# Kernel tuning notes

Measured on AMD Instinct MI355X. Metric: run time of the kernel, lower is better.

The kernel has to match this reference:

```python
import jax, jax.numpy as jnp
import numpy as np
from jax import lax

NUM_HEADS = 8
NUM_SELECTS = 10
CLIP = 10.0  # tanh logit clipping in pointer-style SingleHeadAttention
NEG = -1e9   # finite -inf substitute (safe under autodiff)


def setup_inputs() -> dict:
    key = jax.random.key(0)
    ks = jax.random.split(key, 8)
    B, N, D = 64, 2048, 256
    s = 1.0 / np.sqrt(D)
    return {
        "encoder_output": jax.random.normal(ks[0], (B, N, D), jnp.float32),
        "in_proj_w": jax.random.uniform(ks[1], (3 * D, D), jnp.float32, -s, s),
        "in_proj_b": jnp.zeros((3 * D,), jnp.float32),
        "out_w": jax.random.uniform(ks[2], (D, D), jnp.float32, -s, s),
        "out_b": jnp.zeros((D,), jnp.float32),
        "sha_wq": jax.random.uniform(ks[3], (D, D), jnp.float32, -s, s),
        "sha_wk": jax.random.uniform(ks[4], (D, D), jnp.float32, -s, s),
        "is_training": False,
    }


def reference(encoder_output, in_proj_w, in_proj_b, out_w, out_b, sha_wq, sha_wk, is_training):
    B, N, D = encoder_output.shape
    H, dh, S = NUM_HEADS, D // NUM_HEADS, NUM_SELECTS
    Wq, Wk, Wv = in_proj_w[:D], in_proj_w[D:2 * D], in_proj_w[2 * D:]
    bq, bk, bv = in_proj_b[:D], in_proj_b[D:2 * D], in_proj_b[2 * D:]

    h_mean = jnp.mean(encoder_output, axis=1)                         # [B,D]
    # MHA query is constant across steps; K/V projections of the encoder too.
    q = (h_mean @ Wq.T + bq).reshape(B, H, dh)                        # [B,H,dh]
    k = (encoder_output @ Wk.T + bk).reshape(B, N, H, dh)             # [B,N,H,dh]
    v = (encoder_output @ Wv.T + bv).reshape(B, N, H, dh)             # [B,N,H,dh]
    ksingle = encoder_output @ sha_wk.T                               # [B,N,D]
    scale = 1.0 / np.sqrt(dh)
    scale2 = 1.0 / np.sqrt(D)
    bidx = jnp.arange(B)

    def step(mask, _):
        # multi-head cross attention, key_padding_mask = mask
        s_mha = jnp.einsum('bhd,bnhd->bhn', q, k) * scale             # [B,H,N]
        s_mha = jnp.where(mask[:, None, :], NEG, s_mha)
        a = jax.nn.softmax(s_mha, axis=-1)
        ctx = jnp.einsum('bhn,bnhd->bhd', a, v).reshape(B, D)
        attn_out = ctx @ out_w.T + out_b                              # [B,D]
        # single-head pointer attention with tanh clipping
        qs = attn_out @ sha_wq.T                                      # [B,D]
        u = CLIP * jnp.tanh(jnp.einsum('bd,bnd->bn', qs, ksingle) * scale2)
        u = jnp.where(mask, NEG, u)                                   # [B,N]
        logp = jax.nn.log_softmax(u, axis=-1)
        p = jnp.exp(logp)
        ent = -jnp.sum(jnp.where(p > 0, p * logp, 0.0), axis=-1)
        # is_training=False path: greedy argmax (deterministic reference)
        idx = jnp.argmax(p, axis=-1)                                  # [B]
        pi_s = p[bidx, idx]
        new_mask = mask.at[bidx, idx].set(True)
        return new_mask, (idx, pi_s, ent)

    mask0 = jnp.zeros((B, N), dtype=bool)
    _, (idxs, pis, ents) = lax.scan(step, mask0, None, length=S)
    selected_clients = idxs.T.astype(jnp.int64 if jax.config.jax_enable_x64 else jnp.int32)  # [B,S]
    pi = pis.T                                                        # [B,S]
    entropy = jnp.sum(ents, axis=0)                                   # [B]
    return selected_clients, pi, entropy
```

## Files before the change

kernel.cpp:

```cpp
#include <hip/hip_runtime.h>
#include <hip/hip_bf16.h>
#include <math.h>

namespace {
constexpr int Bc = 64, Nc = 2048, Dc = 256, Hc = 8, DHc = 32, Sc = 10;
constexpr float kNeg = -1000000000.0f;
constexpr float kClip = 10.0f;
constexpr float kScale = 0.17677669529663687f;
constexpr float kScale2 = 0.0625f;
}

__global__ __launch_bounds__(256) void k_hmean_part(const float* __restrict__ enc,
                                                    float* __restrict__ hpart) {
  int b = blockIdx.x >> 5, c = blockIdx.x & 31, d = threadIdx.x;
  const float* p = enc + ((size_t)b * Nc + c * 64) * Dc + d;
  float s = 0.f;
  #pragma unroll 8
  for (int n = 0; n < 64; ++n) s += p[(size_t)n * Dc];
  hpart[(size_t)blockIdx.x * Dc + d] = s;
}

__global__ __launch_bounds__(256) void k_qgc(const float* __restrict__ hpart,
                                             const float* __restrict__ w_in,
                                             const float* __restrict__ b_in,
                                             float* __restrict__ g, float* __restrict__ c) {
  int b = blockIdx.x, t = threadIdx.x;
  __shared__ float hm[Dc];
  __shared__ float qsh[Dc];
  {
    float s = 0.f;
    for (int cc = 0; cc < 32; ++cc) s += hpart[(size_t)(b * 32 + cc) * Dc + t];
    hm[t] = s * (1.0f / Nc);
  }
  __syncthreads();
  {
    const float* row = w_in + (size_t)t * Dc;
    float acc = b_in[t];
    for (int d = 0; d < Dc; ++d) acc += row[d] * hm[d];
    qsh[t] = acc;
  }
  __syncthreads();
  for (int h = 0; h < Hc; ++h) {
    float acc = 0.f;
    const float* wk = w_in + (size_t)(Dc + h * DHc) * Dc + t;
    const float* qh = qsh + h * DHc;
    #pragma unroll 8
    for (int i = 0; i < DHc; ++i) acc += qh[i] * wk[(size_t)i * Dc];
    g[((size_t)b * Hc + h) * Dc + t] = acc;
  }
  if (t < Hc) {
    float acc = 0.f;
    for (int i = 0; i < DHc; ++i) acc += qsh[t * DHc + i] * b_in[Dc + t * DHc + i];
    c[b * Hc + t] = acc;
  }
}

__global__ __launch_bounds__(256) void k_A1(const float* __restrict__ swq,
                                            const float* __restrict__ ow,
                                            const float* __restrict__ ob,
                                            float* __restrict__ M1, float* __restrict__ m1b) {
  int i = blockIdx.x, e = threadIdx.x;
  __shared__ float row[Dc];
  __shared__ float red[256];
  row[e] = swq[(size_t)i * Dc + e];
  __syncthreads();
  float acc = 0.f;
  #pragma unroll 4
  for (int k = 0; k < Dc; ++k) acc += row[k] * ow[(size_t)k * Dc + e];
  M1[(size_t)i * Dc + e] = acc;
  red[e] = row[e] * ob[e];
  __syncthreads();
  for (int off = 128; off >= 1; off >>= 1) {
    if (e < off) red[e] += red[e + off];
    __syncthreads();
  }
  if (e == 0) m1b[i] = red[0];
}

__global__ __launch_bounds__(256) void k_A2(const float* __restrict__ swk,
                                            const float* __restrict__ M1,
                                            const float* __restrict__ m1b,
                                            const float* __restrict__ b_in,
                                            float* __restrict__ Aout, float* __restrict__ cvec) {
  int d = blockIdx.x, e = threadIdx.x;
  __shared__ float col[Dc];
  __shared__ float red[256];
  col[e] = swk[(size_t)e * Dc + d];
  __syncthreads();
  float acc = 0.f;
  #pragma unroll 4
  for (int k = 0; k < Dc; ++k) acc += col[k] * M1[(size_t)k * Dc + e];
  Aout[(size_t)d * Dc + e] = acc;
  red[e] = acc * b_in[2 * Dc + e] + col[e] * m1b[e];
  __syncthreads();
  for (int off = 128; off >= 1; off >>= 1) {
    if (e < off) red[e] += red[e + off];
    __syncthreads();
  }
  if (e == 0) cvec[d] = red[0];
}

__global__ __launch_bounds__(256) void k_A3(const float* __restrict__ Aout,
                                            const float* __restrict__ w_in,
                                            float* __restrict__ BT) {
  int h = blockIdx.x >> 3, et = blockIdx.x & 7, d = threadIdx.x;
  float arow[DHc];
  #pragma unroll
  for (int i = 0; i < DHc; ++i) arow[i] = Aout[(size_t)d * Dc + h * DHc + i];
  __shared__ float wv[DHc][DHc];
  for (int k = threadIdx.x; k < DHc * DHc; k += 256) {
    int i = k >> 5, j = k & 31;
    wv[i][j] = w_in[(size_t)(2 * Dc + h * DHc + i) * Dc + et * DHc + j];
  }
  __syncthreads();
  for (int j = 0; j < DHc; ++j) {
    float acc = 0.f;
    #pragma unroll
    for (int i = 0; i < DHc; ++i) acc += arow[i] * wv[i][j];
    BT[((size_t)h * Dc + et * DHc + j) * Dc + d] = acc;
  }
}

__global__ __launch_bounds__(256) void k_scores(const float* __restrict__ enc,
                                                const float* __restrict__ g,
                                                const float* __restrict__ c,
                                                float* __restrict__ s) {
  int b = blockIdx.x >> 4, nt = blockIdx.x & 15, t = threadIdx.x;
  __shared__ __align__(16) float gsm[Hc * Dc];
  __shared__ float csm[Hc];
  for (int k = t; k < Hc * Dc; k += 256) gsm[k] = g[(size_t)b * Hc * Dc + k];
  if (t < Hc) csm[t] = c[b * Hc + t];
  __syncthreads();
  int row = t >> 1, half = t & 1;
  int n = nt * 128 + row;
  const float4* rowp = reinterpret_cast<const float4*>(enc + ((size_t)b * Nc + n) * Dc);
  float acc[Hc] = {};
  #pragma unroll 8
  for (int i = 0; i < 32; ++i) {
    int d4 = i * 2 + half;
    const float4 e = rowp[d4];
    #pragma unroll
    for (int h = 0; h < Hc; ++h) {
      const float4 g4 = *reinterpret_cast<const float4*>(gsm + h * Dc + d4 * 4);
      acc[h] += e.x * g4.x + e.y * g4.y + e.z * g4.z + e.w * g4.w;
    }
  }
  #pragma unroll
  for (int h = 0; h < Hc; ++h) acc[h] += __shfl_xor(acc[h], 1);
  if (half == 0) {
    #pragma unroll
    for (int h = 0; h < Hc; ++h)
      s[((size_t)b * Hc + h) * Nc + n] = kScale * (acc[h] + csm[h]);
  }
}

__global__ __launch_bounds__(256) void k_rowmax(const float* __restrict__ s,
                                                float* __restrict__ mrow) {
  int bh = blockIdx.x, t = threadIdx.x;
  __shared__ float red[256];
  float m = -3.0e38f;
  #pragma unroll
  for (int q = 0; q < 8; ++q) m = fmaxf(m, s[(size_t)bh * Nc + q * 256 + t]);
  red[t] = m;
  __syncthreads();
  for (int off = 128; off >= 1; off >>= 1) {
    if (t < off) red[t] = fmaxf(red[t], red[t + off]);
    __syncthreads();
  }
  if (t == 0) mrow[bh] = red[0];
}

__global__ __launch_bounds__(256) void k_S0part(const float* __restrict__ enc,
                                                const float* __restrict__ s,
                                                const float* __restrict__ mrow,
                                                float* __restrict__ w,
                                                float* __restrict__ Spart) {
  int b = blockIdx.x >> 3, cid = blockIdx.x & 7, t = threadIdx.x;
  __shared__ float wsm[Hc * 256];
  #pragma unroll
  for (int h = 0; h < Hc; ++h) {
    float m = mrow[b * Hc + h];
    float e = expf(s[((size_t)b * Hc + h) * Nc + cid * 256 + t] - m);
    wsm[h * 256 + t] = e;
    w[((size_t)b * Hc + h) * Nc + cid * 256 + t] = e;
  }
  __syncthreads();
  float acc[Hc] = {};
  const float* ep = enc + ((size_t)b * Nc + cid * 256) * Dc + t;
  for (int ni = 0; ni < 256; ++ni) {
    float ev = ep[(size_t)ni * Dc];
    #pragma unroll
    for (int h = 0; h < Hc; ++h) acc[h] += wsm[h * 256 + ni] * ev;
  }
  #pragma unroll
  for (int h = 0; h < Hc; ++h)
    Spart[(((size_t)b * 8 + cid) * Hc + h) * Dc + t] = acc[h];
}

__global__ __launch_bounds__(256) void k_S0red(const float* __restrict__ Spart,
                                               const float* __restrict__ w,
                                               float* __restrict__ Sacc,
                                               float* __restrict__ W0) {
  int b = blockIdx.x >> 3, h = blockIdx.x & 7, t = threadIdx.x;
  __shared__ float red[256];
  float acc = 0.f;
  for (int cid = 0; cid < 8; ++cid)
    acc += Spart[(((size_t)b * 8 + cid) * Hc + h) * Dc + t];
  Sacc[((size_t)b * Hc + h) * Dc + t] = acc;
  float ws = 0.f;
  #pragma unroll
  for (int q = 0; q < 8; ++q) ws += w[((size_t)b * Hc + h) * Nc + q * 256 + t];
  red[t] = ws;
  __syncthreads();
  for (int off = 128; off >= 1; off >>= 1) {
    if (t < off) red[t] += red[t + off];
    __syncthreads();
  }
  if (t == 0) W0[b * Hc + h] = red[0];
}

__device__ __forceinline__ void select_core(const float* __restrict__ ub,
                                            const int* histsh, int nhist, int t,
                                            float* red, int* redi,
                                            int& gidx_out, float& lse_out, float& ent_out) {
  float uval[8];
  float lmax = -3.0e38f;
  int lidx = 0;
  #pragma unroll
  for (int q = 0; q < 8; ++q) {
    int n = t + q * 256;
    float v = ub[n];
    for (int tt = 0; tt < nhist; ++tt)
      if (n == histsh[tt]) v = kNeg;
    uval[q] = v;
    if (v > lmax) { lmax = v; lidx = n; }
  }
  red[t] = lmax; redi[t] = lidx;
  __syncthreads();
  for (int off = 128; off >= 1; off >>= 1) {
    if (t < off) {
      float o = red[t + off]; int oi = redi[t + off];
      if (o > red[t] || (o == red[t] && oi < redi[t])) { red[t] = o; redi[t] = oi; }
    }
    __syncthreads();
  }
  float mu = red[0];
  int gidx = redi[0];
  __syncthreads();
  float ssum = 0.f;
  #pragma unroll
  for (int q = 0; q < 8; ++q) ssum += expf(uval[q] - mu);
  red[t] = ssum;
  __syncthreads();
  for (int off = 128; off >= 1; off >>= 1) {
    if (t < off) red[t] += red[t + off];
    __syncthreads();
  }
  float Z = red[0];
  float lse = mu + logf(Z);
  __syncthreads();
  float ent = 0.f;
  #pragma unroll
  for (int q = 0; q < 8; ++q) {
    float logp = uval[q] - lse;
    float p = expf(logp);
    if (p > 0.f) ent -= p * logp;
  }
  red[t] = ent;
  __syncthreads();
  for (int off = 128; off >= 1; off >>= 1) {
    if (t < off) red[t] += red[t + off];
    __syncthreads();
  }
  ent_out = red[0];
  gidx_out = gidx;
  lse_out = lse;
  __syncthreads();
}

__global__ __launch_bounds__(256) void k_selchain(const float* __restrict__ u,
                                                  int* __restrict__ hist,
                                                  float* __restrict__ out,
                                                  const float* __restrict__ Sacc,
                                                  const float* __restrict__ W0,
                                                  const float* __restrict__ w,
                                                  const float* __restrict__ enc,
                                                  const float* __restrict__ BT,
                                                  float* __restrict__ rpart, int tstep) {
  int b = blockIdx.x >> 3, h = blockIdx.x & 7, t = threadIdx.x;
  __shared__ float red[256];
  __shared__ int redi[256];
  __shared__ int histsh[16];
  __shared__ float sh[Dc];
  if (t < 16) histsh[t] = (t < tstep - 1) ? hist[b * 16 + t] : -1;
  __syncthreads();

  if (tstep > 0) {
    int sel_t = tstep - 1;
    int gidx; float lse, ent;
    select_core(u + (size_t)b * Nc, histsh, sel_t, t, red, redi, gidx, lse, ent);
    if (h == 0 && t == 0) {
      float pi = expf(u[(size_t)b * Nc + gidx] - lse);
      out[b * Sc + sel_t] = (float)gidx;
      out[Bc * Sc + b * Sc + sel_t] = pi;
      if (sel_t == 0) out[2 * Bc * Sc + b] = ent;
      else out[2 * Bc * Sc + b] += ent;
      hist[b * 16 + sel_t] = gidx;
    }
    if (t == 0) histsh[sel_t] = gidx;
    __syncthreads();
  }

  float se = Sacc[((size_t)b * Hc + h) * Dc + t];
  float Wh = W0[b * Hc + h];
  for (int tt = 0; tt < tstep; ++tt) {
    int j = histsh[tt];
    float wv = w[((size_t)b * Hc + h) * Nc + j];
    se -= wv * enc[((size_t)b * Nc + j) * Dc + t];
    Wh -= wv;
  }
  sh[t] = se / Wh;
  __syncthreads();
  const float* bt = BT + (size_t)h * Dc * Dc + t;
  float a0 = 0.f, a1 = 0.f, a2 = 0.f, a3 = 0.f;
  #pragma unroll 4
  for (int e = 0; e < Dc; e += 4) {
    a0 += bt[(size_t)e * Dc] * sh[e];
    a1 += bt[(size_t)(e + 1) * Dc] * sh[e + 1];
    a2 += bt[(size_t)(e + 2) * Dc] * sh[e + 2];
    a3 += bt[(size_t)(e + 3) * Dc] * sh[e + 3];
  }
  rpart[((size_t)b * Hc + h) * Dc + t] = (a0 + a1) + (a2 + a3);
}

__global__ __launch_bounds__(256) void k_uscore(const float* __restrict__ enc,
                                                const float* __restrict__ rpart,
                                                const float* __restrict__ cvec,
                                                float* __restrict__ u) {
  int b = blockIdx.x >> 5, ng = blockIdx.x & 31, t = threadIdx.x;
  __shared__ __align__(16) float rsm[Dc];
  {
    float vsum = cvec[t];
    #pragma unroll
    for (int h = 0; h < Hc; ++h) vsum += rpart[((size_t)b * Hc + h) * Dc + t];
    rsm[t] = vsum;
  }
  __syncthreads();
  int row = t >> 2, q = t & 3;
  int n = ng * 64 + row;
  const float4* rowp = reinterpret_cast<const float4*>(enc + ((size_t)b * Nc + n) * Dc);
  const float4* r4 = reinterpret_cast<const float4*>(rsm);
  float acc = 0.f;
  #pragma unroll
  for (int i = 0; i < 16; ++i) {
    int d4 = i * 4 + q;
    const float4 e = rowp[d4];
    const float4 rr = r4[d4];
    acc += e.x * rr.x + e.y * rr.y + e.z * rr.z + e.w * rr.w;
  }
  acc += __shfl_xor(acc, 1);
  acc += __shfl_xor(acc, 2);
  if (q == 0) u[(size_t)b * Nc + n] = kClip * tanhf(kScale2 * acc);
}

__global__ __launch_bounds__(256) void k_selfinal(const float* __restrict__ u,
                                                  const int* __restrict__ hist,
                                                  float* __restrict__ out) {
  int b = blockIdx.x, t = threadIdx.x;
  __shared__ float red[256];
  __shared__ int redi[256];
  __shared__ int histsh[16];
  if (t < 16) histsh[t] = (t < Sc - 1) ? hist[b * 16 + t] : -1;
  __syncthreads();
  int gidx; float lse, ent;
  select_core(u + (size_t)b * Nc, histsh, Sc - 1, t, red, redi, gidx, lse, ent);
  if (t == 0) {
    float pi = expf(u[(size_t)b * Nc + gidx] - lse);
    out[b * Sc + (Sc - 1)] = (float)gidx;
    out[Bc * Sc + b * Sc + (Sc - 1)] = pi;
    out[2 * Bc * Sc + b] += ent;
  }
}

extern "C" void kernel_launch(void* const* d_in, const int* in_sizes, int n_in,
                              void* d_out, int out_size, void* d_ws, size_t ws_size,
                              hipStream_t stream) {
  (void)in_sizes; (void)n_in; (void)out_size; (void)ws_size;
  const float* enc  = (const float*)d_in[0];
  const float* in_w = (const float*)d_in[1];
  const float* in_b = (const float*)d_in[2];
  const float* ow   = (const float*)d_in[3];
  const float* ob   = (const float*)d_in[4];
  const float* swq  = (const float*)d_in[5];
  const float* swk  = (const float*)d_in[6];
  float* out = (float*)d_out;

  float* ws = (float*)d_ws;
  size_t off = 0;
  auto alloc = [&](size_t n) { float* p = ws + off; off += n; return p; };
  float* hpart = alloc((size_t)Bc * 32 * Dc);
  float* g     = alloc((size_t)Bc * Hc * Dc);
  float* c     = alloc((size_t)Bc * Hc);
  float* s     = alloc((size_t)Bc * Hc * Nc);
  float* mrow  = alloc((size_t)Bc * Hc);
  float* w     = alloc((size_t)Bc * Hc * Nc);
  float* W0    = alloc((size_t)Bc * Hc);
  float* Spart = alloc((size_t)Bc * 8 * Hc * Dc);
  float* Sacc  = alloc((size_t)Bc * Hc * Dc);
  float* M1    = alloc((size_t)Dc * Dc);
  float* m1b   = alloc(Dc);
  float* Aout  = alloc((size_t)Dc * Dc);
  float* cvec  = alloc(Dc);
  float* BT    = alloc((size_t)Hc * Dc * Dc);
  float* rpart = alloc((size_t)Bc * Hc * Dc);
  float* u     = alloc((size_t)Bc * Nc);
  int* hist    = (int*)alloc((size_t)Bc * 16);

  k_hmean_part<<<Bc * 32, 256, 0, stream>>>(enc, hpart);
  k_qgc<<<Bc, 256, 0, stream>>>(hpart, in_w, in_b, g, c);
  k_A1<<<Dc, 256, 0, stream>>>(swq, ow, ob, M1, m1b);
  k_A2<<<Dc, 256, 0, stream>>>(swk, M1, m1b, in_b, Aout, cvec);
  k_A3<<<Hc * 8, 256, 0, stream>>>(Aout, in_w, BT);
  k_scores<<<Bc * 16, 256, 0, stream>>>(enc, g, c, s);
  k_rowmax<<<Bc * Hc, 256, 0, stream>>>(s, mrow);
  k_S0part<<<Bc * 8, 256, 0, stream>>>(enc, s, mrow, w, Spart);
  k_S0red<<<Bc * Hc, 256, 0, stream>>>(Spart, w, Sacc, W0);

  for (int t = 0; t < Sc; ++t) {
    k_selchain<<<Bc * Hc, 256, 0, stream>>>(u, hist, out, Sacc, W0, w, enc, BT, rpart, t);
    k_uscore<<<Bc * 32, 256, 0, stream>>>(enc, rpart, cvec, u);
  }
  k_selfinal<<<Bc, 256, 0, stream>>>(u, hist, out);
}
```

Baseline: 503.4 us.

## Drop precomputed per-head BT matrix; apply Wv and fused A per batch in selchain

Removes the k_A3 kernel that built an 8x256x256 per-head fused matrix. Instead, each select step does the per-head V projection (Wv rows against the head context) and then a single 256x256 AT multiply per batch, with one block per batch instead of per batch-head. The V bias term moves out of cvec and into ctx. Alongside this, k_S0part and k_uscore are split into twice as many, smaller blocks for more parallelism. The change cuts weight traffic per step (the 2 MB BT is no longer read each step), but the selection loop now runs on only 64 blocks, so the select step runs serially on fewer blocks.

```diff
diff --git a/kernel.cpp b/kernel.cpp
--- a/kernel.cpp
+++ b/kernel.cpp
@@ -80,8 +80,7 @@
 __global__ __launch_bounds__(256) void k_A2(const float* __restrict__ swk,
                                             const float* __restrict__ M1,
                                             const float* __restrict__ m1b,
-                                            const float* __restrict__ b_in,
-                                            float* __restrict__ Aout, float* __restrict__ cvec) {
+                                            float* __restrict__ AT, float* __restrict__ cvec2) {
   int d = blockIdx.x, e = threadIdx.x;
   __shared__ float col[Dc];
   __shared__ float red[256];
@@ -90,35 +89,14 @@
   float acc = 0.f;
   #pragma unroll 4
   for (int k = 0; k < Dc; ++k) acc += col[k] * M1[(size_t)k * Dc + e];
-  Aout[(size_t)d * Dc + e] = acc;
-  red[e] = acc * b_in[2 * Dc + e] + col[e] * m1b[e];
+  AT[(size_t)e * Dc + d] = acc;
+  red[e] = col[e] * m1b[e];
   __syncthreads();
   for (int off = 128; off >= 1; off >>= 1) {
     if (e < off) red[e] += red[e + off];
     __syncthreads();
   }
-  if (e == 0) cvec[d] = red[0];
-}
-
-__global__ __launch_bounds__(256) void k_A3(const float* __restrict__ Aout,
-                                            const float* __restrict__ w_in,
-                                            float* __restrict__ BT) {
-  int h = blockIdx.x >> 3, et = blockIdx.x & 7, d = threadIdx.x;
-  float arow[DHc];
-  #pragma unroll
-  for (int i = 0; i < DHc; ++i) arow[i] = Aout[(size_t)d * Dc + h * DHc + i];
-  __shared__ float wv[DHc][DHc];
-  for (int k = threadIdx.x; k < DHc * DHc; k += 256) {
-    int i = k >> 5, j = k & 31;
-    wv[i][j] = w_in[(size_t)(2 * Dc + h * DHc + i) * Dc + et * DHc + j];
-  }
-  __syncthreads();
-  for (int j = 0; j < DHc; ++j) {
-    float acc = 0.f;
-    #pragma unroll
-    for (int i = 0; i < DHc; ++i) acc += arow[i] * wv[i][j];
-    BT[((size_t)h * Dc + et * DHc + j) * Dc + d] = acc;
-  }
+  if (e == 0) cvec2[d] = red[0];
 }
 
 __global__ __launch_bounds__(256) void k_scores(const float* __restrict__ enc,
@@ -175,26 +153,26 @@
                                                 const float* __restrict__ mrow,
                                                 float* __restrict__ w,
                                                 float* __restrict__ Spart) {
-  int b = blockIdx.x >> 3, cid = blockIdx.x & 7, t = threadIdx.x;
-  __shared__ float wsm[Hc * 256];
-  #pragma unroll
-  for (int h = 0; h < Hc; ++h) {
+  int b = blockIdx.x >> 4, cid = blockIdx.x & 15, t = threadIdx.x;
+  __shared__ float wsm[Hc * 128];
+  for (int k = t; k < Hc * 128; k += 256) {
+    int h = k >> 7, ni = k & 127;
     float m = mrow[b * Hc + h];
-    float e = expf(s[((size_t)b * Hc + h) * Nc + cid * 256 + t] - m);
-    wsm[h * 256 + t] = e;
-    w[((size_t)b * Hc + h) * Nc + cid * 256 + t] = e;
+    float e = expf(s[((size_t)b * Hc + h) * Nc + cid * 128 + ni] - m);
+    wsm[k] = e;
+    w[((size_t)b * Hc + h) * Nc + cid * 128 + ni] = e;
   }
   __syncthreads();
   float acc[Hc] = {};
-  const float* ep = enc + ((size_t)b * Nc + cid * 256) * Dc + t;
-  for (int ni = 0; ni < 256; ++ni) {
+  const float* ep = enc + ((size_t)b * Nc + cid * 128) * Dc + t;
+  for (int ni = 0; ni < 128; ++ni) {
     float ev = ep[(size_t)ni * Dc];
     #pragma unroll
-    for (int h = 0; h < Hc; ++h) acc[h] += wsm[h * 256 + ni] * ev;
+    for (int h = 0; h < Hc; ++h) acc[h] += wsm[h * 128 + ni] * ev;
   }
   #pragma unroll
   for (int h = 0; h < Hc; ++h)
-    Spart[(((size_t)b * 8 + cid) * Hc + h) * Dc + t] = acc[h];
+    Spart[(((size_t)b * 16 + cid) * Hc + h) * Dc + t] = acc[h];
 }
 
 __global__ __launch_bounds__(256) void k_S0red(const float* __restrict__ Spart,
@@ -204,8 +182,8 @@
   int b = blockIdx.x >> 3, h = blockIdx.x & 7, t = threadIdx.x;
   __shared__ float red[256];
   float acc = 0.f;
-  for (int cid = 0; cid < 8; ++cid)
-    acc += Spart[(((size_t)b * 8 + cid) * Hc + h) * Dc + t];
+  for (int cid = 0; cid < 16; ++cid)
+    acc += Spart[(((size_t)b * 16 + cid) * Hc + h) * Dc + t];
   Sacc[((size_t)b * Hc + h) * Dc + t] = acc;
   float ws = 0.f;
   #pragma unroll
@@ -285,81 +263,98 @@
                                                   const float* __restrict__ W0,
                                                   const float* __restrict__ w,
                                                   const float* __restrict__ enc,
-                                                  const float* __restrict__ BT,
-                                                  float* __restrict__ rpart, int tstep) {
-  int b = blockIdx.x >> 3, h = blockIdx.x & 7, t = threadIdx.x;
+                                                  const float* __restrict__ w_in,
+                                                  const float* __restrict__ b_in,
+                                                  const float* __restrict__ AT,
+                                                  const float* __restrict__ cvec2,
+                                                  float* __restrict__ r, int ts) {
+  int b = blockIdx.x, t = threadIdx.x;
   __shared__ float red[256];
   __shared__ int redi[256];
   __shared__ int histsh[16];
-  __shared__ float sh[Dc];
-  if (t < 16) histsh[t] = (t < tstep - 1) ? hist[b * 16 + t] : -1;
-  __syncthreads();
-
-  if (tstep > 0) {
-    int sel_t = tstep - 1;
+  __shared__ float sh[Hc * Dc];
+  __shared__ float ctx[Dc];
+  if (t < 16) histsh[t] = (t < ts - 1) ? hist[b * 16 + t] : -1;
+  __syncthreads();
+
+  if (ts > 0) {
+    int sel_t = ts - 1;
     int gidx; float lse, ent;
     select_core(u + (size_t)b * Nc, histsh, sel_t, t, red, redi, gidx, lse, ent);
-    if (h == 0 && t == 0) {
+    if (t == 0) {
       float pi = expf(u[(size_t)b * Nc + gidx] - lse);
       out[b * Sc + sel_t] = (float)gidx;
       out[Bc * Sc + b * Sc + sel_t] = pi;
       if (sel_t == 0) out[2 * Bc * Sc + b] = ent;
       else out[2 * Bc * Sc + b] += ent;
       hist[b * 16 + sel_t] = gidx;
+      histsh[sel_t] = gidx;
     }
-    if (t == 0) histsh[sel_t] = gidx;
-    __syncthreads();
-  }
-
-  float se = Sacc[((size_t)b * Hc + h) * Dc + t];
-  float Wh = W0[b * Hc + h];
-  for (int tt = 0; tt < tstep; ++tt) {
-    int j = histsh[tt];
-    float wv = w[((size_t)b * Hc + h) * Nc + j];
-    se -= wv * enc[((size_t)b * Nc + j) * Dc + t];
-    Wh -= wv;
-  }
-  sh[t] = se / Wh;
-  __syncthreads();
-  const float* bt = BT + (size_t)h * Dc * Dc + t;
-  float a0 = 0.f, a1 = 0.f, a2 = 0.f, a3 = 0.f;
-  #pragma unroll 4
-  for (int e = 0; e < Dc; e += 4) {
-    a0 += bt[(size_t)e * Dc] * sh[e];
-    a1 += bt[(size_t)(e + 1) * Dc] * sh[e + 1];
-    a2 += bt[(size_t)(e + 2) * Dc] * sh[e + 2];
-    a3 += bt[(size_t)(e + 3) * Dc] * sh[e + 3];
-  }
-  rpart[((size_t)b * Hc + h) * Dc + t] = (a0 + a1) + (a2 + a3);
+    __syncthreads();
+  }
+
+  #pragma unroll
+  for (int h = 0; h < Hc; ++h) {
+    float se = Sacc[((size_t)b * Hc + h) * Dc + t];
+    float Wh = W0[b * Hc + h];
+    for (int tt = 0; tt < ts; ++tt) {
+      int j = histsh[tt];
+      float wv = w[((size_t)b * Hc + h) * Nc + j];
+      se -= wv * enc[((size_t)b * Nc + j) * Dc + t];
+      Wh -= wv;
+    }
+    sh[h * Dc + t] = se / Wh;
+  }
+  __syncthreads();
+
+  {
+    int h2 = t >> 5;
+    const float4* row = reinterpret_cast<const float4*>(w_in + (size_t)(2 * Dc + t) * Dc);
+    const float* shh = sh + h2 * Dc;
+    float a0 = 0.f, a1 = 0.f, a2 = 0.f, a3 = 0.f;
+    #pragma unroll 8
+    for (int d4 = 0; d4 < 64; ++d4) {
+      const float4 rr = row[d4];
+      a0 += rr.x * shh[d4 * 4 + 0];
+      a1 += rr.y * shh[d4 * 4 + 1];
+      a2 += rr.z * shh[d4 * 4 + 2];
+      a3 += rr.w * shh[d4 * 4 + 3];
+    }
+    ctx[t] = (a0 + a1) + (a2 + a3) + b_in[2 * Dc + t];
+  }
+  __syncthreads();
+
+  {
+    float acc = cvec2[t];
+    const float* at = AT + t;
+    #pragma unroll 8
+    for (int k = 0; k < Dc; ++k) acc += at[(size_t)k * Dc] * ctx[k];
+    r[b * Dc + t] = acc;
+  }
 }
 
 __global__ __launch_bounds__(256) void k_uscore(const float* __restrict__ enc,
-                                                const float* __restrict__ rpart,
-                                                const float* __restrict__ cvec,
+                                                const float* __restrict__ r,
                                                 float* __restrict__ u) {
-  int b = blockIdx.x >> 5, ng = blockIdx.x & 31, t = threadIdx.x;
+  int b = blockIdx.x >> 6, ng = blockIdx.x & 63, t = threadIdx.x;
   __shared__ __align__(16) float rsm[Dc];
-  {
-    float vsum = cvec[t];
-    #pragma unroll
-    for (int h = 0; h < Hc; ++h) vsum += rpart[((size_t)b * Hc + h) * Dc + t];
-    rsm[t] = vsum;
-  }
-  __syncthreads();
-  int row = t >> 2, q = t & 3;
-  int n = ng * 64 + row;
+  rsm[t] = r[b * Dc + t];
+  __syncthreads();
+  int row = t >> 3, q = t & 7;
+  int n = ng * 32 + row;
   const float4* rowp = reinterpret_cast<const float4*>(enc + ((size_t)b * Nc + n) * Dc);
   const float4* r4 = reinterpret_cast<const float4*>(rsm);
   float acc = 0.f;
   #pragma unroll
-  for (int i = 0; i < 16; ++i) {
-    int d4 = i * 4 + q;
+  for (int i = 0; i < 8; ++i) {
+    int d4 = i * 8 + q;
     const float4 e = rowp[d4];
     const float4 rr = r4[d4];
     acc += e.x * rr.x + e.y * rr.y + e.z * rr.z + e.w * rr.w;
   }
   acc += __shfl_xor(acc, 1);
   acc += __shfl_xor(acc, 2);
+  acc += __shfl_xor(acc, 4);
   if (q == 0) u[(size_t)b * Nc + n] = kClip * tanhf(kScale2 * acc);
 }
 
@@ -405,30 +400,29 @@
   float* mrow  = alloc((size_t)Bc * Hc);
   float* w     = alloc((size_t)Bc * Hc * Nc);
   float* W0    = alloc((size_t)Bc * Hc);
-  float* Spart = alloc((size_t)Bc * 8 * Hc * Dc);
+  float* Spart = alloc((size_t)Bc * 16 * Hc * Dc);
   float* Sacc  = alloc((size_t)Bc * Hc * Dc);
   float* M1    = alloc((size_t)Dc * Dc);
   float* m1b   = alloc(Dc);
-  float* Aout  = alloc((size_t)Dc * Dc);
-  float* cvec  = alloc(Dc);
-  float* BT    = alloc((size_t)Hc * Dc * Dc);
-  float* rpart = alloc((size_t)Bc * Hc * Dc);
+  float* AT    = alloc((size_t)Dc * Dc);
+  float* cvec2 = alloc(Dc);
+  float* r     = alloc((size_t)Bc * Dc);
   float* u     = alloc((size_t)Bc * Nc);
   int* hist    = (int*)alloc((size_t)Bc * 16);
 
   k_hmean_part<<<Bc * 32, 256, 0, stream>>>(enc, hpart);
   k_qgc<<<Bc, 256, 0, stream>>>(hpart, in_w, in_b, g, c);
   k_A1<<<Dc, 256, 0, stream>>>(swq, ow, ob, M1, m1b);
-  k_A2<<<Dc, 256, 0, stream>>>(swk, M1, m1b, in_b, Aout, cvec);
-  k_A3<<<Hc * 8, 256, 0, stream>>>(Aout, in_w, BT);
+  k_A2<<<Dc, 256, 0, stream>>>(swk, M1, m1b, AT, cvec2);
   k_scores<<<Bc * 16, 256, 0, stream>>>(enc, g, c, s);
   k_rowmax<<<Bc * Hc, 256, 0, stream>>>(s, mrow);
-  k_S0part<<<Bc * 8, 256, 0, stream>>>(enc, s, mrow, w, Spart);
+  k_S0part<<<Bc * 16, 256, 0, stream>>>(enc, s, mrow, w, Spart);
   k_S0red<<<Bc * Hc, 256, 0, stream>>>(Spart, w, Sacc, W0);
 
   for (int t = 0; t < Sc; ++t) {
-    k_selchain<<<Bc * Hc, 256, 0, stream>>>(u, hist, out, Sacc, W0, w, enc, BT, rpart, t);
-    k_uscore<<<Bc * 32, 256, 0, stream>>>(enc, rpart, cvec, u);
+    k_selchain<<<Bc, 256, 0, stream>>>(u, hist, out, Sacc, W0, w, enc,
+                                       in_w, in_b, AT, cvec2, r, t);
+    k_uscore<<<Bc * 64, 256, 0, stream>>>(enc, r, u);
   }
   k_selfinal<<<Bc, 256, 0, stream>>>(u, hist, out);
 }
```

Result: slower. 671.8 us (+33.5%).
